# Performance work log

Hardware: AMD Instinct MI355X
Metric: run time of the kernel (lower is better)

Reference implementation:

```python
import jax, jax.numpy as jnp
import numpy as np

DIM = 1024
N_QUAT = DIM // 4
LN_EPS = 1e-5
NORM_EPS = 1e-12


def quat_mul(q1, q2):
    # q1, q2: [B, L, N, 4]
    r1, i1, j1, k1 = q1[..., 0], q1[..., 1], q1[..., 2], q1[..., 3]
    r2, i2, j2, k2 = q2[..., 0], q2[..., 1], q2[..., 2], q2[..., 3]
    r = r1 * r2 - i1 * i2 - j1 * j2 - k1 * k2
    i = r1 * i2 + i1 * r2 + j1 * k2 - k1 * j2
    j = r1 * j2 - i1 * k2 + j1 * r2 + k1 * i2
    k = r1 * k2 + i1 * j2 - j1 * i2 + k1 * r2
    return jnp.stack([r, i, j, k], axis=-1)


def quat_conj(q):
    return q * jnp.array([1.0, -1.0, -1.0, -1.0], dtype=q.dtype)


def setup_inputs() -> dict:
    key = jax.random.key(0)
    ks = jax.random.split(key, 7)
    B, L, D = 4, 4096, DIM
    s = 1.0 / np.sqrt(D)
    return {
        "x": jax.random.normal(ks[0], (B, L, D), dtype=jnp.float32),
        "Wk": jax.random.normal(ks[1], (D, D), dtype=jnp.float32) * s,
        "bk": jnp.zeros((D,), dtype=jnp.float32),
        "Wv": jax.random.normal(ks[2], (D, D), dtype=jnp.float32) * s,
        "bv": jnp.zeros((D,), dtype=jnp.float32),
        "ln_g": jnp.ones((D,), dtype=jnp.float32),
        "ln_b": jnp.zeros((D,), dtype=jnp.float32),
        "Wo": jax.random.normal(ks[3], (D, D), dtype=jnp.float32) * s,
        "bo": jnp.zeros((D,), dtype=jnp.float32),
    }


def reference(x, Wk, bk, Wv, bv, ln_g, ln_b, Wo, bo):
    B, L, D = x.shape
    keys = (x @ Wk.T + bk).reshape(B, L, N_QUAT, 4)
    knorm = jnp.linalg.norm(keys, axis=-1, keepdims=True)
    keys = keys / jnp.maximum(knorm, NORM_EPS)  # F.normalize
    values = (x @ Wv.T + bv).reshape(B, L, N_QUAT, 4)
    bound = quat_mul(values, keys)
    memory = jnp.cumsum(bound, axis=1)
    retrieved = quat_mul(memory, quat_conj(keys)).reshape(B, L, D)
    positions = jnp.arange(1, L + 1, dtype=x.dtype)
    retrieved = retrieved / jnp.sqrt(positions)[None, :, None]
    # LayerNorm over last dim
    mu = jnp.mean(retrieved, axis=-1, keepdims=True)
    var = jnp.var(retrieved, axis=-1, keepdims=True)
    normed = (retrieved - mu) / jnp.sqrt(var + LN_EPS) * ln_g + ln_b
    return x + (normed @ Wo.T + bo)
```

## Files before the change

kernel.cpp:

```cpp
#include <hip/hip_runtime.h>
#include <cstdint>
#include <cstddef>


typedef float    f32x4 __attribute__((ext_vector_type(4)));
typedef _Float16 f16x8 __attribute__((ext_vector_type(8)));
typedef _Float16 f16x4 __attribute__((ext_vector_type(4)));

#define DEV static __device__ __forceinline__

constexpr int BATCH = 4;
constexpr int LSEQ  = 4096;
constexpr int DIMN  = 1024;
constexpr int MROW  = BATCH * LSEQ;
constexpr int SEG   = 128;
constexpr int SL    = LSEQ / SEG;
constexpr int NT    = DIMN / 64;

DEV f32x4 qmul(f32x4 a, f32x4 b) {
  f32x4 r;
  r.x = a.x*b.x - a.y*b.y - a.z*b.z - a.w*b.w;
  r.y = a.x*b.y + a.y*b.x + a.z*b.w - a.w*b.z;
  r.z = a.x*b.z - a.y*b.w + a.z*b.x + a.w*b.y;
  r.w = a.x*b.w + a.y*b.z - a.z*b.y + a.w*b.x;
  return r;
}

DEV f32x4 h2f(f16x4 h) {
  return (f32x4){(float)h.x, (float)h.y, (float)h.z, (float)h.w};
}

__global__ __launch_bounds__(256) void k_cast_f16(const float* __restrict__ in,
                                                  _Float16* __restrict__ out, int n4) {
  int i = blockIdx.x * 256 + threadIdx.x;
  if (i < n4) {
    f32x4 v = ((const f32x4*)in)[i];
    f16x4 o = { (_Float16)v.x, (_Float16)v.y, (_Float16)v.z, (_Float16)v.w };
    ((f16x4*)out)[i] = o;
  }
}

__global__ __launch_bounds__(256) void k_cast_w3(const float* __restrict__ w0,
                                                 const float* __restrict__ w1,
                                                 const float* __restrict__ w2,
                                                 _Float16* __restrict__ out, int n4each) {
  int i = blockIdx.x * 256 + threadIdx.x;
  if (i >= 3 * n4each) return;
  const float* src = (i < n4each) ? w0 : (i < 2 * n4each ? w1 : w2);
  int j = (i < n4each) ? i : (i < 2 * n4each ? i - n4each : i - 2 * n4each);
  f32x4 v = ((const f32x4*)src)[j];
  f16x4 o = { (_Float16)v.x, (_Float16)v.y, (_Float16)v.z, (_Float16)v.w };
  ((f16x4*)out)[i] = o;
}

__global__ __launch_bounds__(512, 2) void k_gemm256(
    const _Float16* __restrict__ A, const _Float16* __restrict__ Bw,
    const float* __restrict__ biasA, const float* __restrict__ biasB, int nsplit,
    _Float16* __restrict__ C, int ldC, int nbn) {
  extern __shared__ char smem[];
  const int tid  = threadIdx.x;
  const int lane = tid & 63;
  const int wid  = tid >> 6;
  const int wr = wid >> 2, wc = wid & 3;

  const int nwg = gridDim.x;
  const int cpx = nwg >> 3;
  const int swz = (blockIdx.x & 7) * cpx + (blockIdx.x >> 3);
  const int bm = swz / nbn, bn = swz % nbn;

  auto regBase = [](int slot, int isB, int half) -> unsigned {
    return (unsigned)(((slot * 2 + isB) * 2 + half) * 16384);
  };
  const int r8    = lane >> 3;
  const int sslot = (lane & 7) ^ r8;
  const char* aT = (const char*)(A  + (size_t)bm * 256 * DIMN);
  const char* bT = (const char*)(Bw + (size_t)bn * 256 * DIMN);

  auto stage = [&](int isB, int half, int slot, int kt) {
    const char* gb = (isB ? bT : aT) + (size_t)(half * 128) * 2048 + kt * 128;
    const unsigned reg = regBase(slot, isB, half);
#pragma unroll
    for (int i = 0; i < 2; ++i) {
      const int c = wid * 2 + i;
      const char* src = gb + (size_t)(c * 8 + r8) * 2048 + (sslot << 4);
      __builtin_amdgcn_global_load_lds(
          (const __attribute__((address_space(1))) void*)src,
          (__attribute__((address_space(3))) void*)(smem + reg + c * 1024), 16, 0, 0);
    }
  };
  auto fragA = [&](int slot, int m, int kk) -> f16x8 {
    const int half = m >> 2;
    const int row  = wr * 64 + (m & 3) * 16 + (lane & 15);
    const int sl   = (kk * 4 + (lane >> 4)) ^ (row & 7);
    return *(const f16x8*)(smem + regBase(slot, 0, half) + row * 128 + (sl << 4));
  };
  auto fragB = [&](int slot, int n, int kk) -> f16x8 {
    const int half = n >> 1;
    const int row  = wc * 32 + (n & 1) * 16 + (lane & 15);
    const int sl   = (kk * 4 + (lane >> 4)) ^ (row & 7);
    return *(const f16x8*)(smem + regBase(slot, 1, half) + row * 128 + (sl << 4));
  };

  f32x4 acc[8][4];
#pragma unroll
  for (int m = 0; m < 8; ++m)
#pragma unroll
    for (int n = 0; n < 4; ++n) acc[m][n] = (f32x4){0.f, 0.f, 0.f, 0.f};

  stage(0, 0, 0, 0); stage(1, 0, 0, 0); stage(0, 1, 0, 0); stage(1, 1, 0, 0);
  asm volatile("s_waitcnt vmcnt(4)" ::: "memory");
  __builtin_amdgcn_s_barrier();

  f16x8 a[4][2], b0[2][2], b1[2][2];
#pragma unroll 2
  for (int T = 0; T < NT; ++T) {
    const int slot = T & 1, ns = slot ^ 1;
    const bool pf = (T + 1 < NT);
    if (pf) {
      stage(0, 0, ns, T + 1); stage(1, 0, ns, T + 1);
      stage(0, 1, ns, T + 1); stage(1, 1, ns, T + 1);
    }
#pragma unroll
    for (int m = 0; m < 4; ++m) { a[m][0] = fragA(slot, m, 0); a[m][1] = fragA(slot, m, 1); }
#pragma unroll
    for (int n = 0; n < 2; ++n) { b0[n][0] = fragB(slot, n, 0); b0[n][1] = fragB(slot, n, 1); }
    if (pf) asm volatile("s_waitcnt vmcnt(8)" ::: "memory");
    else    asm volatile("s_waitcnt vmcnt(0)" ::: "memory");
    __builtin_amdgcn_s_barrier();
    __builtin_amdgcn_s_setprio(1);
#pragma unroll
    for (int m = 0; m < 4; ++m)
#pragma unroll
      for (int n = 0; n < 2; ++n) {
        acc[m][n] = __builtin_amdgcn_mfma_f32_16x16x32_f16(a[m][0], b0[n][0], acc[m][n], 0, 0, 0);
        acc[m][n] = __builtin_amdgcn_mfma_f32_16x16x32_f16(a[m][1], b0[n][1], acc[m][n], 0, 0, 0);
      }
    __builtin_amdgcn_s_setprio(0);
    __builtin_amdgcn_s_barrier();
#pragma unroll
    for (int n = 0; n < 2; ++n) { b1[n][0] = fragB(slot, n + 2, 0); b1[n][1] = fragB(slot, n + 2, 1); }
    __builtin_amdgcn_s_barrier();
    __builtin_amdgcn_s_setprio(1);
#pragma unroll
    for (int m = 0; m < 4; ++m)
#pragma unroll
      for (int n = 0; n < 2; ++n) {
        acc[m][n + 2] = __builtin_amdgcn_mfma_f32_16x16x32_f16(a[m][0], b1[n][0], acc[m][n + 2], 0, 0, 0);
        acc[m][n + 2] = __builtin_amdgcn_mfma_f32_16x16x32_f16(a[m][1], b1[n][1], acc[m][n + 2], 0, 0, 0);
      }
    __builtin_amdgcn_s_setprio(0);
    __builtin_amdgcn_s_barrier();
#pragma unroll
    for (int m = 0; m < 4; ++m) { a[m][0] = fragA(slot, m + 4, 0); a[m][1] = fragA(slot, m + 4, 1); }
    __builtin_amdgcn_s_barrier();
    __builtin_amdgcn_s_setprio(1);
#pragma unroll
    for (int m = 0; m < 4; ++m)
#pragma unroll
      for (int n = 0; n < 2; ++n) {
        acc[m + 4][n] = __builtin_amdgcn_mfma_f32_16x16x32_f16(a[m][0], b0[n][0], acc[m + 4][n], 0, 0, 0);
        acc[m + 4][n] = __builtin_amdgcn_mfma_f32_16x16x32_f16(a[m][1], b0[n][1], acc[m + 4][n], 0, 0, 0);
      }
    __builtin_amdgcn_s_setprio(0);
    __builtin_amdgcn_s_barrier();
    if (pf) asm volatile("s_waitcnt vmcnt(4)" ::: "memory");
    __builtin_amdgcn_s_barrier();
    __builtin_amdgcn_s_setprio(1);
#pragma unroll
    for (int m = 0; m < 4; ++m)
#pragma unroll
      for (int n = 0; n < 2; ++n) {
        acc[m + 4][n + 2] = __builtin_amdgcn_mfma_f32_16x16x32_f16(a[m][0], b1[n][0], acc[m + 4][n + 2], 0, 0, 0);
        acc[m + 4][n + 2] = __builtin_amdgcn_mfma_f32_16x16x32_f16(a[m][1], b1[n][1], acc[m + 4][n + 2], 0, 0, 0);
      }
    __builtin_amdgcn_s_setprio(0);
    __builtin_amdgcn_s_barrier();
  }

  const int r0 = bm * 256 + wr * 64 + ((lane >> 4) << 2);
  const int c0 = bn * 256 + wc * 32 + (lane & 15);
#pragma unroll
  for (int n = 0; n < 4; ++n) {
    const int col = c0 + (n >> 1) * 128 + (n & 1) * 16;
    const float bc = (col < nsplit) ? biasA[col] : biasB[col - nsplit];
#pragma unroll
    for (int m = 0; m < 8; ++m) {
      const int row = r0 + (m >> 2) * 128 + (m & 3) * 16;
#pragma unroll
      for (int t = 0; t < 4; ++t) {
        C[(size_t)(row + t) * ldC + col] = (_Float16)(acc[m][n][t] + bc);
      }
    }
  }
}

__global__ __launch_bounds__(512, 2) void k_gemm_out(
    const _Float16* __restrict__ A, const _Float16* __restrict__ Bw,
    const float* __restrict__ bias, const _Float16* __restrict__ residH,
    float* __restrict__ C, int nbn) {
  extern __shared__ char smem[];
  const int tid  = threadIdx.x;
  const int lane = tid & 63;
  const int wid  = tid >> 6;
  const int wr = wid >> 2, wc = wid & 3;

  const int nwg = gridDim.x;
  const int cpx = nwg >> 3;
  const int swz = (blockIdx.x & 7) * cpx + (blockIdx.x >> 3);
  const int bm = swz / nbn, bn = swz % nbn;

  const int r8    = lane >> 3;
  const int sslot = (lane & 7) ^ r8;
  const char* aT = (const char*)(A  + (size_t)bm * 128 * DIMN);
  const char* bT = (const char*)(Bw + (size_t)bn * 256 * DIMN);

  auto stage3 = [&](int slot, int kt) {
    char* base = smem + slot * 49152;
#pragma unroll
    for (int i = 0; i < 2; ++i) {
      const int c = wid * 2 + i;
      const char* src = aT + kt * 128 + (size_t)(c * 8 + r8) * 2048 + (sslot << 4);
      __builtin_amdgcn_global_load_lds(
          (const __attribute__((address_space(1))) void*)src,
          (__attribute__((address_space(3))) void*)(base + c * 1024), 16, 0, 0);
    }
#pragma unroll
    for (int i = 0; i < 4; ++i) {
      const int c = wid * 4 + i;
      const char* src = bT + kt * 128 + (size_t)(c * 8 + r8) * 2048 + (sslot << 4);
      __builtin_amdgcn_global_load_lds(
          (const __attribute__((address_space(1))) void*)src,
          (__attribute__((address_space(3))) void*)(base + 16384 + c * 1024), 16, 0, 0);
    }
  };
  auto fragA = [&](int slot, int m, int kk) -> f16x8 {
    const int row = wr * 64 + m * 16 + (lane & 15);
    const int sl  = (kk * 4 + (lane >> 4)) ^ (row & 7);
    return *(const f16x8*)(smem + slot * 49152 + row * 128 + (sl << 4));
  };
  auto fragB = [&](int slot, int n, int kk) -> f16x8 {
    const int row = (n >> 1) * 128 + wc * 32 + (n & 1) * 16 + (lane & 15);
    const int sl  = (kk * 4 + (lane >> 4)) ^ (row & 7);
    return *(const f16x8*)(smem + slot * 49152 + 16384 + row * 128 + (sl << 4));
  };

  f32x4 acc[4][4];
#pragma unroll
  for (int m = 0; m < 4; ++m)
#pragma unroll
    for (int n = 0; n < 4; ++n) acc[m][n] = (f32x4){0.f, 0.f, 0.f, 0.f};

  stage3(0, 0); stage3(1, 1);
  asm volatile("s_waitcnt vmcnt(6)" ::: "memory");
  __builtin_amdgcn_s_barrier();

  f16x8 a[4][2], b0[2][2], b1[2][2];
#pragma unroll 2
  for (int T = 0; T < NT; ++T) {
    const int s = T % 3, sw = (T + 2) % 3;
    if (T + 2 < NT) stage3(sw, T + 2);
#pragma unroll
    for (int m = 0; m < 4; ++m) { a[m][0] = fragA(s, m, 0); a[m][1] = fragA(s, m, 1); }
#pragma unroll
    for (int n = 0; n < 2; ++n) { b0[n][0] = fragB(s, n, 0); b0[n][1] = fragB(s, n, 1); }
    __builtin_amdgcn_s_barrier();
    __builtin_amdgcn_s_setprio(1);
#pragma unroll
    for (int m = 0; m < 4; ++m)
#pragma unroll
      for (int n = 0; n < 2; ++n) {
        acc[m][n] = __builtin_amdgcn_mfma_f32_16x16x32_f16(a[m][0], b0[n][0], acc[m][n], 0, 0, 0);
        acc[m][n] = __builtin_amdgcn_mfma_f32_16x16x32_f16(a[m][1], b0[n][1], acc[m][n], 0, 0, 0);
      }
    __builtin_amdgcn_s_setprio(0);
    __builtin_amdgcn_s_barrier();
#pragma unroll
    for (int n = 0; n < 2; ++n) { b1[n][0] = fragB(s, n + 2, 0); b1[n][1] = fragB(s, n + 2, 1); }
    if (T < NT - 2)       asm volatile("s_waitcnt vmcnt(6)" ::: "memory");
    else if (T == NT - 2) asm volatile("s_waitcnt vmcnt(0)" ::: "memory");
    __builtin_amdgcn_s_barrier();
    __builtin_amdgcn_s_setprio(1);
#pragma unroll
    for (int m = 0; m < 4; ++m)
#pragma unroll
      for (int n = 0; n < 2; ++n) {
        acc[m][n + 2] = __builtin_amdgcn_mfma_f32_16x16x32_f16(a[m][0], b1[n][0], acc[m][n + 2], 0, 0, 0);
        acc[m][n + 2] = __builtin_amdgcn_mfma_f32_16x16x32_f16(a[m][1], b1[n][1], acc[m][n + 2], 0, 0, 0);
      }
    __builtin_amdgcn_s_setprio(0);
    __builtin_amdgcn_s_barrier();
  }

  const int r0 = bm * 128 + wr * 64 + ((lane >> 4) << 2);
  const int c0 = bn * 256 + wc * 32 + (lane & 15);
#pragma unroll
  for (int n = 0; n < 4; ++n) {
    const int col = c0 + (n >> 1) * 128 + (n & 1) * 16;
    const float bc = bias[col];
#pragma unroll
    for (int m = 0; m < 4; ++m) {
      const int row = r0 + m * 16;
#pragma unroll
      for (int t = 0; t < 4; ++t) {
        const size_t off = (size_t)(row + t) * DIMN + col;
        C[off] = acc[m][n][t] + bc + (float)residH[off];
      }
    }
  }
}

__global__ __launch_bounds__(256) void k_segsum(const _Float16* __restrict__ KVh,
                                                float* __restrict__ segsum) {
  const int b = blockIdx.x >> 7, seg = blockIdx.x & 127, n = threadIdx.x;
  f32x4 ssum = (f32x4){0.f, 0.f, 0.f, 0.f};
  const size_t rb = (size_t)(b * LSEQ + seg * SL) * 2048 + n * 4;
  for (int l = 0; l < SL; ++l) {
    const size_t p = rb + (size_t)l * 2048;
    f32x4 kq = h2f(*(const f16x4*)(KVh + p));
    f32x4 vq = h2f(*(const f16x4*)(KVh + p + 1024));
    float nn = sqrtf(kq.x*kq.x + kq.y*kq.y + kq.z*kq.z + kq.w*kq.w);
    f32x4 kh = kq * (1.0f / fmaxf(nn, 1e-12f));
    ssum += qmul(vq, kh);
  }
  ((f32x4*)segsum)[(size_t)blockIdx.x * 256 + n] = ssum;
}

__global__ __launch_bounds__(256) void k_segscan(const float* __restrict__ segsum,
                                                 float* __restrict__ segoff) {
  const int gt = blockIdx.x * 256 + threadIdx.x;
  const int b = gt >> 10, ch = gt & 1023;
  float run = 0.f;
  for (int s = 0; s < SEG; ++s) {
    const size_t idx = ((size_t)(b * SEG + s)) * 1024 + ch;
    float v = segsum[idx];
    segoff[idx] = run;
    run += v;
  }
}

__global__ __launch_bounds__(256) void k_retrieve_ln(
    const _Float16* __restrict__ KVh, const float* __restrict__ segoff,
    const float* __restrict__ g, const float* __restrict__ bb,
    _Float16* __restrict__ out) {
  const int b = blockIdx.x >> 7, seg = blockIdx.x & 127, n = threadIdx.x;
  const int wid = n >> 6, lane = n & 63;
  __shared__ float p1[2][4], p2[2][4];
  f32x4 mem = ((const f32x4*)segoff)[(size_t)blockIdx.x * 256 + n];
  const f32x4 gg  = ((const f32x4*)g)[n];
  const f32x4 bvv = ((const f32x4*)bb)[n];
  const size_t rb = (size_t)(b * LSEQ + seg * SL) * 2048 + n * 4;
  const int grow = b * LSEQ + seg * SL;

  f16x4 kq = *(const f16x4*)(KVh + rb);
  f16x4 vq = *(const f16x4*)(KVh + rb + 1024);
  for (int l = 0; l < SL; ++l) {
    f16x4 kqn, vqn;
    if (l + 1 < SL) {
      kqn = *(const f16x4*)(KVh + rb + (size_t)(l + 1) * 2048);
      vqn = *(const f16x4*)(KVh + rb + (size_t)(l + 1) * 2048 + 1024);
    }
    f32x4 kf = h2f(kq), vf = h2f(vq);
    float nn = sqrtf(kf.x*kf.x + kf.y*kf.y + kf.z*kf.z + kf.w*kf.w);
    f32x4 kh = kf * (1.0f / fmaxf(nn, 1e-12f));
    mem += qmul(vf, kh);
    f32x4 kc = (f32x4){kh.x, -kh.y, -kh.z, -kh.w};
    f32x4 r = qmul(mem, kc);
    r *= rsqrtf((float)(seg * SL + l + 1));

    float s1 = r.x + r.y + r.z + r.w;
    float s2 = r.x*r.x + r.y*r.y + r.z*r.z + r.w*r.w;
#pragma unroll
    for (int off = 32; off > 0; off >>= 1) {
      s1 += __shfl_down(s1, off, 64);
      s2 += __shfl_down(s2, off, 64);
    }
    if (lane == 0) { p1[l & 1][wid] = s1; p2[l & 1][wid] = s2; }
    __syncthreads();
    const float ts1 = p1[l & 1][0] + p1[l & 1][1] + p1[l & 1][2] + p1[l & 1][3];
    const float ts2 = p2[l & 1][0] + p2[l & 1][1] + p2[l & 1][2] + p2[l & 1][3];
    const float mu = ts1 * (1.0f / 1024.0f);
    const float var = ts2 * (1.0f / 1024.0f) - mu * mu;
    const float rstd = rsqrtf(var + 1e-5f);
    f32x4 nv = (r - mu) * rstd * gg + bvv;
    f16x4 o = { (_Float16)nv.x, (_Float16)nv.y, (_Float16)nv.z, (_Float16)nv.w };
    ((f16x4*)out)[(size_t)(grow + l) * 256 + n] = o;
    kq = kqn; vq = vqn;
  }
}

extern "C" void kernel_launch(void* const* d_in, const int* in_sizes, int n_in,
                              void* d_out, int out_size, void* d_ws, size_t ws_size,
                              hipStream_t stream) {
  const float* x    = (const float*)d_in[0];
  const float* Wk   = (const float*)d_in[1];
  const float* bk   = (const float*)d_in[2];
  const float* Wv   = (const float*)d_in[3];
  const float* bv   = (const float*)d_in[4];
  const float* ln_g = (const float*)d_in[5];
  const float* ln_b = (const float*)d_in[6];
  const float* Wo   = (const float*)d_in[7];
  const float* bo   = (const float*)d_in[8];
  float* out = (float*)d_out;

  char* ws = (char*)d_ws;
  size_t off = 0;
  auto alloc = [&](size_t bytes) -> void* {
    void* p = ws + off;
    off += (bytes + 255) & ~(size_t)255;
    return p;
  };
  _Float16* xb   = (_Float16*)alloc((size_t)MROW * DIMN * 2);
  _Float16* wkvb = (_Float16*)alloc((size_t)3 * DIMN * DIMN * 2);
  _Float16* KVh  = (_Float16*)alloc((size_t)MROW * 2 * DIMN * 2);
  float* segsum  = (float*)alloc((size_t)BATCH * SEG * DIMN * 4);
  float* segoff  = (float*)alloc((size_t)BATCH * SEG * DIMN * 4);
  _Float16* nb   = (_Float16*)alloc((size_t)MROW * DIMN * 2);
  _Float16* wob  = wkvb + (size_t)2 * DIMN * DIMN;
  (void)off; (void)ws_size; (void)in_sizes; (void)n_in; (void)out_size;

  hipFuncSetAttribute((const void*)k_gemm256,
                      hipFuncAttributeMaxDynamicSharedMemorySize, 131072);
  hipFuncSetAttribute((const void*)k_gemm_out,
                      hipFuncAttributeMaxDynamicSharedMemorySize, 147456);

  k_cast_f16<<<MROW * DIMN / 4 / 256, 256, 0, stream>>>(x, xb, MROW * DIMN / 4);
  k_cast_w3<<<3 * DIMN * DIMN / 4 / 256, 256, 0, stream>>>(Wk, Wv, Wo, wkvb, DIMN * DIMN / 4);

  k_gemm256<<<(MROW / 256) * (2048 / 256), 512, 131072, stream>>>(
      xb, wkvb, bk, bv, 1024, KVh, 2048, 2048 / 256);

  k_segsum<<<BATCH * SEG, 256, 0, stream>>>(KVh, segsum);
  k_segscan<<<BATCH * DIMN / 256, 256, 0, stream>>>(segsum, segoff);
  k_retrieve_ln<<<BATCH * SEG, 256, 0, stream>>>(KVh, segoff, ln_g, ln_b, nb);

  k_gemm_out<<<(MROW / 128) * (DIMN / 256), 512, 147456, stream>>>(
      nb, wob, bo, xb, out, DIMN / 256);
}
```

Baseline: 207.2 us.

## Simplify GEMM main loops to one barrier phase and merge cast kernels

Both MFMA GEMM kernels drop their interleaved multi-barrier schedule. Each iteration now waits on vmcnt, hits one barrier, loads all A and B fragments, then runs the MFMAs with a single trailing barrier. This cuts per-iteration barrier overhead, but loses the finer overlap of LDS reads with MFMA work and raises register pressure. The two fp32-to-fp16 cast kernels are also merged into one launch, which relies on the weight buffer sitting directly after the x buffer in the workspace.

Result: no change. 209.8 us (+1.2%).

```diff
diff --git a/kernel.cpp b/kernel.cpp
--- a/kernel.cpp
+++ b/kernel.cpp
@@ -30,24 +30,19 @@
   return (f32x4){(float)h.x, (float)h.y, (float)h.z, (float)h.w};
 }
 
-__global__ __launch_bounds__(256) void k_cast_f16(const float* __restrict__ in,
-                                                  _Float16* __restrict__ out, int n4) {
+__global__ __launch_bounds__(256) void k_cast_all(
+    const float* __restrict__ x, const float* __restrict__ w0,
+    const float* __restrict__ w1, const float* __restrict__ w2,
+    _Float16* __restrict__ out) {
+  const int XN4 = MROW * DIMN / 4;
+  const int WN4 = DIMN * DIMN / 4;
   int i = blockIdx.x * 256 + threadIdx.x;
-  if (i < n4) {
-    f32x4 v = ((const f32x4*)in)[i];
-    f16x4 o = { (_Float16)v.x, (_Float16)v.y, (_Float16)v.z, (_Float16)v.w };
-    ((f16x4*)out)[i] = o;
-  }
-}
-
-__global__ __launch_bounds__(256) void k_cast_w3(const float* __restrict__ w0,
-                                                 const float* __restrict__ w1,
-                                                 const float* __restrict__ w2,
-                                                 _Float16* __restrict__ out, int n4each) {
-  int i = blockIdx.x * 256 + threadIdx.x;
-  if (i >= 3 * n4each) return;
-  const float* src = (i < n4each) ? w0 : (i < 2 * n4each ? w1 : w2);
-  int j = (i < n4each) ? i : (i < 2 * n4each ? i - n4each : i - 2 * n4each);
+  if (i >= XN4 + 3 * WN4) return;
+  const float* src; int j;
+  if (i < XN4)                { src = x;  j = i; }
+  else if (i < XN4 + WN4)     { src = w0; j = i - XN4; }
+  else if (i < XN4 + 2 * WN4) { src = w1; j = i - XN4 - WN4; }
+  else                        { src = w2; j = i - XN4 - 2 * WN4; }
   f32x4 v = ((const f32x4*)src)[j];
   f16x4 o = { (_Float16)v.x, (_Float16)v.y, (_Float16)v.z, (_Float16)v.w };
   ((f16x4*)out)[i] = o;
@@ -108,10 +103,8 @@
     for (int n = 0; n < 4; ++n) acc[m][n] = (f32x4){0.f, 0.f, 0.f, 0.f};
 
   stage(0, 0, 0, 0); stage(1, 0, 0, 0); stage(0, 1, 0, 0); stage(1, 1, 0, 0);
-  asm volatile("s_waitcnt vmcnt(4)" ::: "memory");
-  __builtin_amdgcn_s_barrier();
-
-  f16x8 a[4][2], b0[2][2], b1[2][2];
+
+  f16x8 a[4][2], b[4][2];
 #pragma unroll 2
   for (int T = 0; T < NT; ++T) {
     const int slot = T & 1, ns = slot ^ 1;
@@ -119,59 +112,35 @@
     if (pf) {
       stage(0, 0, ns, T + 1); stage(1, 0, ns, T + 1);
       stage(0, 1, ns, T + 1); stage(1, 1, ns, T + 1);
-    }
+      asm volatile("s_waitcnt vmcnt(8)" ::: "memory");
+    } else {
+      asm volatile("s_waitcnt vmcnt(0)" ::: "memory");
+    }
+    __builtin_amdgcn_s_barrier();
+
 #pragma unroll
     for (int m = 0; m < 4; ++m) { a[m][0] = fragA(slot, m, 0); a[m][1] = fragA(slot, m, 1); }
 #pragma unroll
-    for (int n = 0; n < 2; ++n) { b0[n][0] = fragB(slot, n, 0); b0[n][1] = fragB(slot, n, 1); }
-    if (pf) asm volatile("s_waitcnt vmcnt(8)" ::: "memory");
-    else    asm volatile("s_waitcnt vmcnt(0)" ::: "memory");
-    __builtin_amdgcn_s_barrier();
+    for (int n = 0; n < 4; ++n) { b[n][0] = fragB(slot, n, 0); b[n][1] = fragB(slot, n, 1); }
     __builtin_amdgcn_s_setprio(1);
 #pragma unroll
     for (int m = 0; m < 4; ++m)
 #pragma unroll
-      for (int n = 0; n < 2; ++n) {
-        acc[m][n] = __builtin_amdgcn_mfma_f32_16x16x32_f16(a[m][0], b0[n][0], acc[m][n], 0, 0, 0);
-        acc[m][n] = __builtin_amdgcn_mfma_f32_16x16x32_f16(a[m][1], b0[n][1], acc[m][n], 0, 0, 0);
+      for (int n = 0; n < 4; ++n) {
+        acc[m][n] = __builtin_amdgcn_mfma_f32_16x16x32_f16(a[m][0], b[n][0], acc[m][n], 0, 0, 0);
+        acc[m][n] = __builtin_amdgcn_mfma_f32_16x16x32_f16(a[m][1], b[n][1], acc[m][n], 0, 0, 0);
       }
     __builtin_amdgcn_s_setprio(0);
-    __builtin_amdgcn_s_barrier();
-#pragma unroll
-    for (int n = 0; n < 2; ++n) { b1[n][0] = fragB(slot, n + 2, 0); b1[n][1] = fragB(slot, n + 2, 1); }
-    __builtin_amdgcn_s_barrier();
+
+#pragma unroll
+    for (int m = 0; m < 4; ++m) { a[m][0] = fragA(slot, m + 4, 0); a[m][1] = fragA(slot, m + 4, 1); }
     __builtin_amdgcn_s_setprio(1);
 #pragma unroll
     for (int m = 0; m < 4; ++m)
 #pragma unroll
-      for (int n = 0; n < 2; ++n) {
-        acc[m][n + 2] = __builtin_amdgcn_mfma_f32_16x16x32_f16(a[m][0], b1[n][0], acc[m][n + 2], 0, 0, 0);
-        acc[m][n + 2] = __builtin_amdgcn_mfma_f32_16x16x32_f16(a[m][1], b1[n][1], acc[m][n + 2], 0, 0, 0);
-      }
-    __builtin_amdgcn_s_setprio(0);
-    __builtin_amdgcn_s_barrier();
-#pragma unroll
-    for (int m = 0; m < 4; ++m) { a[m][0] = fragA(slot, m + 4, 0); a[m][1] = fragA(slot, m + 4, 1); }
-    __builtin_amdgcn_s_barrier();
-    __builtin_amdgcn_s_setprio(1);
-#pragma unroll
-    for (int m = 0; m < 4; ++m)
-#pragma unroll
-      for (int n = 0; n < 2; ++n) {
-        acc[m + 4][n] = __builtin_amdgcn_mfma_f32_16x16x32_f16(a[m][0], b0[n][0], acc[m + 4][n], 0, 0, 0);
-        acc[m + 4][n] = __builtin_amdgcn_mfma_f32_16x16x32_f16(a[m][1], b0[n][1], acc[m + 4][n], 0, 0, 0);
-      }
-    __builtin_amdgcn_s_setprio(0);
-    __builtin_amdgcn_s_barrier();
-    if (pf) asm volatile("s_waitcnt vmcnt(4)" ::: "memory");
-    __builtin_amdgcn_s_barrier();
-    __builtin_amdgcn_s_setprio(1);
-#pragma unroll
-    for (int m = 0; m < 4; ++m)
-#pragma unroll
-      for (int n = 0; n < 2; ++n) {
-        acc[m + 4][n + 2] = __builtin_amdgcn_mfma_f32_16x16x32_f16(a[m][0], b1[n][0], acc[m + 4][n + 2], 0, 0, 0);
-        acc[m + 4][n + 2] = __builtin_amdgcn_mfma_f32_16x16x32_f16(a[m][1], b1[n][1], acc[m + 4][n + 2], 0, 0, 0);
+      for (int n = 0; n < 4; ++n) {
+        acc[m + 4][n] = __builtin_amdgcn_mfma_f32_16x16x32_f16(a[m][0], b[n][0], acc[m + 4][n], 0, 0, 0);
+        acc[m + 4][n] = __builtin_amdgcn_mfma_f32_16x16x32_f16(a[m][1], b[n][1], acc[m + 4][n], 0, 0, 0);
       }
     __builtin_amdgcn_s_setprio(0);
     __builtin_amdgcn_s_barrier();
@@ -251,41 +220,28 @@
     for (int n = 0; n < 4; ++n) acc[m][n] = (f32x4){0.f, 0.f, 0.f, 0.f};
 
   stage3(0, 0); stage3(1, 1);
-  asm volatile("s_waitcnt vmcnt(6)" ::: "memory");
-  __builtin_amdgcn_s_barrier();
-
-  f16x8 a[4][2], b0[2][2], b1[2][2];
-#pragma unroll 2
+
+  f16x8 a[4][2], b[4][2];
   for (int T = 0; T < NT; ++T) {
     const int s = T % 3, sw = (T + 2) % 3;
-    if (T + 2 < NT) stage3(sw, T + 2);
+    if (T + 2 < NT) {
+      stage3(sw, T + 2);
+      asm volatile("s_waitcnt vmcnt(6)" ::: "memory");
+    } else {
+      asm volatile("s_waitcnt vmcnt(0)" ::: "memory");
+    }
+    __builtin_amdgcn_s_barrier();
 #pragma unroll
     for (int m = 0; m < 4; ++m) { a[m][0] = fragA(s, m, 0); a[m][1] = fragA(s, m, 1); }
 #pragma unroll
-    for (int n = 0; n < 2; ++n) { b0[n][0] = fragB(s, n, 0); b0[n][1] = fragB(s, n, 1); }
-    __builtin_amdgcn_s_barrier();
+    for (int n = 0; n < 4; ++n) { b[n][0] = fragB(s, n, 0); b[n][1] = fragB(s, n, 1); }
     __builtin_amdgcn_s_setprio(1);
 #pragma unroll
     for (int m = 0; m < 4; ++m)
 #pragma unroll
-      for (int n = 0; n < 2; ++n) {
-        acc[m][n] = __builtin_amdgcn_mfma_f32_16x16x32_f16(a[m][0], b0[n][0], acc[m][n], 0, 0, 0);
-        acc[m][n] = __builtin_amdgcn_mfma_f32_16x16x32_f16(a[m][1], b0[n][1], acc[m][n], 0, 0, 0);
-      }
-    __builtin_amdgcn_s_setprio(0);
-    __builtin_amdgcn_s_barrier();
-#pragma unroll
-    for (int n = 0; n < 2; ++n) { b1[n][0] = fragB(s, n + 2, 0); b1[n][1] = fragB(s, n + 2, 1); }
-    if (T < NT - 2)       asm volatile("s_waitcnt vmcnt(6)" ::: "memory");
-    else if (T == NT - 2) asm volatile("s_waitcnt vmcnt(0)" ::: "memory");
-    __builtin_amdgcn_s_barrier();
-    __builtin_amdgcn_s_setprio(1);
-#pragma unroll
-    for (int m = 0; m < 4; ++m)
-#pragma unroll
-      for (int n = 0; n < 2; ++n) {
-        acc[m][n + 2] = __builtin_amdgcn_mfma_f32_16x16x32_f16(a[m][0], b1[n][0], acc[m][n + 2], 0, 0, 0);
-        acc[m][n + 2] = __builtin_amdgcn_mfma_f32_16x16x32_f16(a[m][1], b1[n][1], acc[m][n + 2], 0, 0, 0);
+      for (int n = 0; n < 4; ++n) {
+        acc[m][n] = __builtin_amdgcn_mfma_f32_16x16x32_f16(a[m][0], b[n][0], acc[m][n], 0, 0, 0);
+        acc[m][n] = __builtin_amdgcn_mfma_f32_16x16x32_f16(a[m][1], b[n][1], acc[m][n], 0, 0, 0);
       }
     __builtin_amdgcn_s_setprio(0);
     __builtin_amdgcn_s_barrier();
@@ -423,8 +379,8 @@
   hipFuncSetAttribute((const void*)k_gemm_out,
                       hipFuncAttributeMaxDynamicSharedMemorySize, 147456);
 
-  k_cast_f16<<<MROW * DIMN / 4 / 256, 256, 0, stream>>>(x, xb, MROW * DIMN / 4);
-  k_cast_w3<<<3 * DIMN * DIMN / 4 / 256, 256, 0, stream>>>(Wk, Wv, Wo, wkvb, DIMN * DIMN / 4);
+  const int castN4 = MROW * DIMN / 4 + 3 * DIMN * DIMN / 4;
+  k_cast_all<<<(castN4 + 255) / 256, 256, 0, stream>>>(x, Wk, Wv, Wo, xb);
 
   k_gemm256<<<(MROW / 256) * (2048 / 256), 512, 131072, stream>>>(
       xb, wkvb, bk, bv, 1024, KVh, 2048, 2048 / 256);
```
